# Kernel tuning notes

Measured on AMD Instinct MI355X. Metric: run time of the kernel, lower is better.

The kernel has to match this reference:

```python
import jax, jax.numpy as jnp
import numpy as np

K_BITS = 8
D_V = 32

# 256-entry popcount lookup table (float, matching torch buffer)
_POP_LUT = jnp.asarray(np.array([bin(i).count('1') for i in range(256)], dtype=np.float32))


def setup_inputs() -> dict:
    key = jax.random.key(0)
    k1, k2, k3 = jax.random.split(key, 3)
    B, H, W = 8, 64, 64
    z = jax.random.uniform(k1, (B, K_BITS, H, W), dtype=jnp.float32)
    temperature = jnp.asarray(1.0, dtype=jnp.float32)
    value_embed = jax.random.normal(k2, (256, D_V), dtype=jnp.float32)  # nn.Embedding default N(0,1)
    return {"z": z, "temperature": temperature, "value_embed": value_embed}


def reference(z, temperature, value_embed):
    B, k, H, W = z.shape
    N = H * W
    d_v = value_embed.shape[1]
    # bitpack: threshold to {0,1}, pack k bits into one byte code per position
    bits = (z > 0.5).astype(jnp.int32)                       # (B,k,H,W)
    shifts = (2 ** jnp.arange(k, dtype=jnp.int32)).reshape(1, k, 1, 1)
    codes = (bits * shifts).sum(axis=1).reshape(B, N)        # (B,N) in [0,255]
    # pairwise Hamming distance via XOR + LUT popcount
    xor = codes[:, :, None] ^ codes[:, None, :]              # (B,N,N) int
    dist = _POP_LUT[xor]                                     # (B,N,N) float
    scores = -dist / jnp.clip(temperature, 0.1)
    attn = jax.nn.softmax(scores, axis=-1)                   # (B,N,N)
    values = value_embed[jnp.clip(codes, 0, 255)]            # (B,N,d_v)
    ctx = jnp.einsum('bnm,bmd->bnd', attn, values)           # (B,N,d_v)
    return ctx.transpose(0, 2, 1).reshape(B, d_v, H, W)
```

## Files before the change

kernel.cpp:

```cpp
#include <hip/hip_runtime.h>
#include <hip/hip_bf16.h>

#define B_SZ   8
#define KBITS  8
#define NPOS   4096
#define DV     32
#define NCODE  256
#define PARTS  4

__global__ __launch_bounds__(256) void k_codes_hist(const float* __restrict__ z,
                                                    unsigned char* __restrict__ codes,
                                                    int* __restrict__ hist) {
    const int b = blockIdx.x >> 2;
    const int p = blockIdx.x & (PARTS - 1);
    __shared__ int h[NCODE];
    h[threadIdx.x] = 0;
    __syncthreads();

    const float* zb = z + (size_t)b * KBITS * NPOS;
    const int base = p * (NPOS / PARTS);
    for (int i = threadIdx.x; i < NPOS / PARTS; i += 256) {
        const int n = base + i;
        int code = 0;
#pragma unroll
        for (int bit = 0; bit < KBITS; ++bit)
            code |= (zb[bit * NPOS + n] > 0.5f) ? (1 << bit) : 0;
        codes[b * NPOS + n] = (unsigned char)code;
        atomicAdd(&h[code], 1);
    }
    __syncthreads();
    hist[blockIdx.x * NCODE + threadIdx.x] = h[threadIdx.x];
}

__global__ __launch_bounds__(256) void k_table(const int* __restrict__ hist,
                                               const float* __restrict__ V,
                                               const float* __restrict__ temp,
                                               float* __restrict__ Ttab) {
    const int bid = blockIdx.x;
    const int b   = bid >> 5;
    const int dch = (bid >> 2) & 7;
    const int cch = bid & 3;

    __shared__ float Vld[NCODE * 4];
    __shared__ float cntf[NCODE];
    __shared__ float wl[KBITS + 1];

    const int tid = threadIdx.x;
    for (int idx = tid; idx < NCODE * 4; idx += 256) {
        const int v = idx >> 2, j = idx & 3;
        Vld[idx] = V[v * DV + dch * 4 + j];
    }
    {
        int s = 0;
#pragma unroll
        for (int p = 0; p < PARTS; ++p)
            s += hist[(b * PARTS + p) * NCODE + tid];
        cntf[tid] = (float)s;
    }
    if (tid <= KBITS) {
        const float Tc = fmaxf(temp[0], 0.1f);
        wl[tid] = expf(-(float)tid / Tc);
    }
    __syncthreads();

    const int c  = cch * 64 + (tid & 63);
    const int dl = tid >> 6;
    float accS = 0.f, accV = 0.f;
#pragma unroll 8
    for (int v = 0; v < NCODE; ++v) {
        const float cw = cntf[v] * wl[__popc(c ^ v)];
        accS += cw;
        accV = fmaf(cw, Vld[v * 4 + dl], accV);
    }
    const int d = dch * 4 + dl;
    Ttab[((b * DV + d) * NCODE) + c] = accV / accS;
}

__global__ __launch_bounds__(256) void k_out(const unsigned char* __restrict__ codes,
                                             const float* __restrict__ Ttab,
                                             float* __restrict__ out) {
    const int b = blockIdx.x >> 5;
    const int d = blockIdx.x & 31;
    __shared__ float tab[NCODE];
    tab[threadIdx.x] = Ttab[((b * DV + d) * NCODE) + threadIdx.x];
    __syncthreads();

    const uchar4* c4 = (const uchar4*)(codes + (size_t)b * NPOS);
    float4* o4 = (float4*)(out + (size_t)(b * DV + d) * NPOS);
    for (int i = threadIdx.x; i < NPOS / 4; i += 256) {
        const uchar4 cc = c4[i];
        float4 r;
        r.x = tab[cc.x];
        r.y = tab[cc.y];
        r.z = tab[cc.z];
        r.w = tab[cc.w];
        o4[i] = r;
    }
}

extern "C" void kernel_launch(void* const* d_in, const int* in_sizes, int n_in,
                              void* d_out, int out_size, void* d_ws, size_t ws_size,
                              hipStream_t stream) {
    const float* z    = (const float*)d_in[0];
    const float* temp = (const float*)d_in[1];
    const float* V    = (const float*)d_in[2];
    float* out        = (float*)d_out;

    char* ws = (char*)d_ws;
    unsigned char* codes = (unsigned char*)ws;
    int*   hist = (int*)(ws + B_SZ * NPOS);
    float* Ttab = (float*)(ws + B_SZ * NPOS + B_SZ * PARTS * NCODE * 4);

    k_codes_hist<<<B_SZ * PARTS, 256, 0, stream>>>(z, codes, hist);
    k_table<<<B_SZ * 8 * 4, 256, 0, stream>>>(hist, V, temp, Ttab);
    k_out<<<B_SZ * DV, 256, 0, stream>>>(codes, Ttab, out);
}
```

Measured before the change: 72.40 us.

## Fuse code/hist/table/output into one kernel with Walsh-style butterfly table transform

Replaces the three-kernel pipeline with one kernel per (batch, slice). Each block recomputes the batch's codes and histogram in shared memory. It then builds the Hamming-weighted table with an 8-stage butterfly transform, exploiting the factorization exp(-popc/T) = prod a^bit, instead of the 256x256 direct sum. This removes two launches and the global round trips. In exchange, each of the 32 slice blocks redundantly reads the full batch's z and recomputes the table.

```diff
diff --git a/kernel.cpp b/kernel.cpp
--- a/kernel.cpp
+++ b/kernel.cpp
@@ -6,95 +6,84 @@
 #define NPOS   4096
 #define DV     32
 #define NCODE  256
-#define PARTS  4
+#define NSLICE 32
 
-__global__ __launch_bounds__(256) void k_codes_hist(const float* __restrict__ z,
-                                                    unsigned char* __restrict__ codes,
-                                                    int* __restrict__ hist) {
-    const int b = blockIdx.x >> 2;
-    const int p = blockIdx.x & (PARTS - 1);
+__global__ __launch_bounds__(1024) void k_fused(const float* __restrict__ z,
+                                                const float* __restrict__ V,
+                                                const float* __restrict__ temp,
+                                                float* __restrict__ out) {
+    const int b = blockIdx.x >> 5;
+    const int s = blockIdx.x & (NSLICE - 1);
+    const int tid = threadIdx.x;
+
+    __shared__ unsigned int codes_u[NPOS / 4];
     __shared__ int h[NCODE];
-    h[threadIdx.x] = 0;
+    __shared__ float T[NCODE][DV + 1];
+
+    if (tid < NCODE) h[tid] = 0;
     __syncthreads();
 
-    const float* zb = z + (size_t)b * KBITS * NPOS;
-    const int base = p * (NPOS / PARTS);
-    for (int i = threadIdx.x; i < NPOS / PARTS; i += 256) {
-        const int n = base + i;
-        int code = 0;
+    {
+        const float4* z4 = (const float4*)(z + (size_t)b * KBITS * NPOS);
+        unsigned int c0 = 0, c1 = 0, c2 = 0, c3 = 0;
 #pragma unroll
-        for (int bit = 0; bit < KBITS; ++bit)
-            code |= (zb[bit * NPOS + n] > 0.5f) ? (1 << bit) : 0;
-        codes[b * NPOS + n] = (unsigned char)code;
-        atomicAdd(&h[code], 1);
-    }
-    __syncthreads();
-    hist[blockIdx.x * NCODE + threadIdx.x] = h[threadIdx.x];
-}
-
-__global__ __launch_bounds__(256) void k_table(const int* __restrict__ hist,
-                                               const float* __restrict__ V,
-                                               const float* __restrict__ temp,
-                                               float* __restrict__ Ttab) {
-    const int bid = blockIdx.x;
-    const int b   = bid >> 5;
-    const int dch = (bid >> 2) & 7;
-    const int cch = bid & 3;
-
-    __shared__ float Vld[NCODE * 4];
-    __shared__ float cntf[NCODE];
-    __shared__ float wl[KBITS + 1];
-
-    const int tid = threadIdx.x;
-    for (int idx = tid; idx < NCODE * 4; idx += 256) {
-        const int v = idx >> 2, j = idx & 3;
-        Vld[idx] = V[v * DV + dch * 4 + j];
-    }
-    {
-        int s = 0;
-#pragma unroll
-        for (int p = 0; p < PARTS; ++p)
-            s += hist[(b * PARTS + p) * NCODE + tid];
-        cntf[tid] = (float)s;
-    }
-    if (tid <= KBITS) {
-        const float Tc = fmaxf(temp[0], 0.1f);
-        wl[tid] = expf(-(float)tid / Tc);
+        for (int bit = 0; bit < KBITS; ++bit) {
+            const float4 f = z4[bit * (NPOS / 4) + tid];
+            c0 |= (unsigned)(f.x > 0.5f) << bit;
+            c1 |= (unsigned)(f.y > 0.5f) << bit;
+            c2 |= (unsigned)(f.z > 0.5f) << bit;
+            c3 |= (unsigned)(f.w > 0.5f) << bit;
+        }
+        codes_u[tid] = c0 | (c1 << 8) | (c2 << 16) | (c3 << 24);
+        atomicAdd(&h[c0], 1);
+        atomicAdd(&h[c1], 1);
+        atomicAdd(&h[c2], 1);
+        atomicAdd(&h[c3], 1);
     }
     __syncthreads();
 
-    const int c  = cch * 64 + (tid & 63);
-    const int dl = tid >> 6;
-    float accS = 0.f, accV = 0.f;
-#pragma unroll 8
-    for (int v = 0; v < NCODE; ++v) {
-        const float cw = cntf[v] * wl[__popc(c ^ v)];
-        accS += cw;
-        accV = fmaf(cw, Vld[v * 4 + dl], accV);
+    for (int idx = tid; idx < NCODE * DV; idx += 1024) {
+        const int v = idx >> 5, d = idx & 31;
+        T[v][d] = (float)h[v] * V[v * DV + d];
     }
-    const int d = dch * 4 + dl;
-    Ttab[((b * DV + d) * NCODE) + c] = accV / accS;
-}
+    if (tid < NCODE) T[tid][DV] = (float)h[tid];
 
-__global__ __launch_bounds__(256) void k_out(const unsigned char* __restrict__ codes,
-                                             const float* __restrict__ Ttab,
-                                             float* __restrict__ out) {
-    const int b = blockIdx.x >> 5;
-    const int d = blockIdx.x & 31;
-    __shared__ float tab[NCODE];
-    tab[threadIdx.x] = Ttab[((b * DV + d) * NCODE) + threadIdx.x];
+    const float a = expf(-1.0f / fmaxf(temp[0], 0.1f));
+#pragma unroll 1
+    for (int st = 0; st < KBITS; ++st) {
+        __syncthreads();
+        for (int i = tid; i < (DV + 1) * 128; i += 1024) {
+            const int c = i >> 7;
+            const int p = i & 127;
+            const int lo = p & ((1 << st) - 1);
+            const int v0 = ((p >> st) << (st + 1)) | lo;
+            const int v1 = v0 | (1 << st);
+            const float t0 = T[v0][c], t1 = T[v1][c];
+            T[v0][c] = fmaf(a, t1, t0);
+            T[v1][c] = fmaf(a, t0, t1);
+        }
+    }
     __syncthreads();
 
-    const uchar4* c4 = (const uchar4*)(codes + (size_t)b * NPOS);
-    float4* o4 = (float4*)(out + (size_t)(b * DV + d) * NPOS);
-    for (int i = threadIdx.x; i < NPOS / 4; i += 256) {
-        const uchar4 cc = c4[i];
-        float4 r;
-        r.x = tab[cc.x];
-        r.y = tab[cc.y];
-        r.z = tab[cc.z];
-        r.w = tab[cc.w];
-        o4[i] = r;
+    if (tid < NCODE) T[tid][DV] = 1.0f / T[tid][DV];
+    __syncthreads();
+    for (int idx = tid; idx < NCODE * DV; idx += 1024) {
+        const int v = idx >> 5, d = idx & 31;
+        T[v][d] *= T[v][DV];
+    }
+    __syncthreads();
+
+    {
+        const unsigned char* cbytes = (const unsigned char*)codes_u;
+        const int nl = tid & 127;
+        const int dg = tid >> 7;
+        const int code = cbytes[s * 128 + nl];
+        float* ob = out + (size_t)(b * DV) * NPOS + s * 128 + nl;
+#pragma unroll
+        for (int j = 0; j < 4; ++j) {
+            const int d = dg + 8 * j;
+            ob[(size_t)d * NPOS] = T[code][d];
+        }
     }
 }
 
@@ -106,12 +95,5 @@
     const float* V    = (const float*)d_in[2];
     float* out        = (float*)d_out;
 
-    char* ws = (char*)d_ws;
-    unsigned char* codes = (unsigned char*)ws;
-    int*   hist = (int*)(ws + B_SZ * NPOS);
-    float* Ttab = (float*)(ws + B_SZ * NPOS + B_SZ * PARTS * NCODE * 4);
-
-    k_codes_hist<<<B_SZ * PARTS, 256, 0, stream>>>(z, codes, hist);
-    k_table<<<B_SZ * 8 * 4, 256, 0, stream>>>(hist, V, temp, Ttab);
-    k_out<<<B_SZ * DV, 256, 0, stream>>>(codes, Ttab, out);
+    k_fused<<<B_SZ * NSLICE, 1024, 0, stream>>>(z, V, temp, out);
 }
```

Measured after the change: 66.06 us. 8.7% less time.
